# Optimization experiments

Measured on AMD Instinct MI355X. Metric: run time of the kernel, lower is better.

Reference implementation:

```python
import jax, jax.numpy as jnp
import numpy as np

B, S, H, I, E, TOP_K = 2, 1024, 1024, 2048, 8, 2


def setup_inputs() -> dict:
    key = jax.random.key(0)
    ks = jax.random.split(key, 5)
    return {
        "hidden_states": jax.random.normal(ks[0], (B, S, H), jnp.float32),
        # torch Linear weights are (out, in)
        "router_w": jax.random.normal(ks[1], (E, H), jnp.float32) * 0.02,
        "w1": jax.random.normal(ks[2], (E, I, H), jnp.float32) * 0.02,
        "v": jax.random.normal(ks[3], (E, I, H), jnp.float32) * 0.02,
        "w2": jax.random.normal(ks[4], (E, H, I), jnp.float32) * 0.02,
    }


def _moe(x, router_w, w1, v, w2):
    # x: [T, H] flattened tokens
    T = x.shape[0]
    n_exp = router_w.shape[0]
    logits = x @ router_w.T                                    # [T, E]
    probs = jax.nn.softmax(logits.astype(jnp.float32), axis=-1)
    top_p, top_i = jax.lax.top_k(probs, TOP_K)                 # [T, K]
    top_p = top_p / top_p.sum(axis=-1, keepdims=True)
    top_p = top_p.astype(x.dtype)
    # dense gate matrix [T, E]; zero for unselected experts -> identical math
    # to the torch gather / index_add combine
    gates = jnp.zeros((T, n_exp), x.dtype).at[
        jnp.arange(T)[:, None], top_i].set(top_p)
    out = jnp.zeros_like(x)
    for e in range(n_exp):  # small fixed expert loop keeps peak memory low
        h = jax.nn.gelu(x @ w1[e].T, approximate=False) * (x @ v[e].T)  # [T, I]
        out = out + gates[:, e:e + 1] * (h @ w2[e].T)                   # [T, H]
    return out, logits


def reference(hidden_states, router_w, w1, v, w2):
    b, s, h = hidden_states.shape
    out, logits = _moe(hidden_states.reshape(-1, h), router_w, w1, v, w2)
    return out.reshape(b, s, h), logits
```

## Files before the change

### kernel.cpp

```cpp
#include <hip/hip_runtime.h>
#include <math.h>

#define T 2048
#define HD 1024
#define ID 2048
#define NE 8
#define CSTRIDE 32

typedef short bf16x8 __attribute__((ext_vector_type(8)));
typedef float f32x4 __attribute__((ext_vector_type(4)));
typedef unsigned short u16x4 __attribute__((ext_vector_type(4)));
typedef unsigned short u16x8 __attribute__((ext_vector_type(8)));

__device__ __forceinline__ unsigned short f2bf(float f) {
  union { float f; unsigned u; } v; v.f = f;
  unsigned r = v.u + 0x7FFFu + ((v.u >> 16) & 1u);
  return (unsigned short)(r >> 16);
}

__device__ __forceinline__ u16x8 cvt8(float4 a, float4 b) {
  u16x8 o;
  o[0] = f2bf(a.x); o[1] = f2bf(a.y); o[2] = f2bf(a.z); o[3] = f2bf(a.w);
  o[4] = f2bf(b.x); o[5] = f2bf(b.y); o[6] = f2bf(b.z); o[7] = f2bf(b.w);
  return o;
}

__device__ __forceinline__ void cast_chunk16(const float* __restrict__ s,
                                             unsigned short* __restrict__ d,
                                             size_t base) {
  size_t o = base + (size_t)threadIdx.x * 4;
#pragma unroll
  for (int k = 0; k < 4; k++) {
    float4 f = *(const float4*)(s + o + k * 1024);
    u16x4 h;
    h[0] = f2bf(f.x); h[1] = f2bf(f.y); h[2] = f2bf(f.z); h[3] = f2bf(f.w);
    *(u16x4*)(d + o + k * 1024) = h;
  }
}

__device__ __forceinline__ void glds16(const unsigned short* g, unsigned short* l) {
  __builtin_amdgcn_global_load_lds(
      (const __attribute__((address_space(1))) unsigned int*)(g),
      (__attribute__((address_space(3))) unsigned int*)(l), 16, 0, 0);
}

__global__ __launch_bounds__(256) void prep_kernel(
    const float* __restrict__ x, const float* __restrict__ rw,
    unsigned short* __restrict__ xb, float* __restrict__ logits_out,
    int* __restrict__ pair_rowid, float* __restrict__ pair_gate,
    int* __restrict__ counts) {
  int bx = blockIdx.x;
  if (bx >= 256) {
    cast_chunk16(x, xb, (size_t)(bx - 256) * 4096);
    return;
  }
  __shared__ int s_e[16];
  __shared__ int s_rid[16];
  __shared__ float s_gt[16];
  int tid = threadIdx.x;
  int wid = tid >> 6, lane = tid & 63;
  for (int tk = 0; tk < 2; ++tk) {
    int t = bx * 8 + wid * 2 + tk;
    float acc[NE];
#pragma unroll
    for (int e = 0; e < NE; e++) acc[e] = 0.f;
    const float* xrow = x + (size_t)t * HD;
#pragma unroll 2
    for (int j = 0; j < HD; j += 64) {
      float xv = xrow[j + lane];
#pragma unroll
      for (int e = 0; e < NE; e++) acc[e] += xv * rw[e * HD + j + lane];
    }
#pragma unroll
    for (int e = 0; e < NE; e++)
      for (int off = 32; off > 0; off >>= 1) acc[e] += __shfl_xor(acc[e], off, 64);
    if (lane == 0) {
#pragma unroll
      for (int e = 0; e < NE; e++) logits_out[t * NE + e] = acc[e];
      int e0 = 0;
#pragma unroll
      for (int e = 1; e < NE; e++) if (acc[e] > acc[e0]) e0 = e;
      int e1 = (e0 == 0) ? 1 : 0;
#pragma unroll
      for (int e = 0; e < NE; e++)
        if (e != e0 && e != e1 && acc[e] > acc[e1]) e1 = e;
      float b = __expf(acc[e1] - acc[e0]);
      float g0 = 1.f / (1.f + b);
      float g1 = 1.f - g0;
      int slot = (wid * 2 + tk) * 2;
      s_e[slot] = e0; s_rid[slot] = t * 2;     s_gt[slot] = g0;
      s_e[slot + 1] = e1; s_rid[slot + 1] = t * 2 + 1; s_gt[slot + 1] = g1;
    }
  }
  __syncthreads();
  if (tid < NE) {
    int cnt = 0;
#pragma unroll
    for (int k = 0; k < 16; k++) if (s_e[k] == tid) cnt++;
    if (cnt) {
      int base = atomicAdd(&counts[tid * CSTRIDE], cnt);
      int p = 0;
      for (int k = 0; k < 16; k++)
        if (s_e[k] == tid) {
          pair_rowid[tid * T + base + p] = s_rid[k];
          pair_gate[tid * T + base + p] = s_gt[k];
          p++;
        }
    }
  }
}

__global__ __launch_bounds__(256) void gemm1_kernel(
    const unsigned short* __restrict__ xb, const float* __restrict__ w1,
    const float* __restrict__ v, unsigned short* __restrict__ hb,
    const int* __restrict__ pair_rowid, const int* __restrict__ counts) {
  int e = blockIdx.z;
  int cnt = counts[e * CSTRIDE];
  int row0 = blockIdx.y * 128;
  if (row0 >= cnt) return;
  __shared__ unsigned short As[2][128 * 64];
  __shared__ unsigned short B1s[2][64 * 64];
  __shared__ unsigned short B2s[2][64 * 64];
  int tid = threadIdx.x;
  int lane = tid & 63, wid = tid >> 6;
  int wr = wid >> 1, wc = wid & 1;
  int col0 = blockIdx.x * 64;
  int gr = lane >> 3, gc = lane & 7;
  const unsigned short *aA[4];
  const float *aB1[2], *aB2[2];
#pragma unroll
  for (int c = 0; c < 4; c++) {
    int row = (c * 4 + wid) * 8 + gr;
    int idx = row0 + row; if (idx > cnt - 1) idx = cnt - 1;
    int tok = pair_rowid[e * T + idx] >> 1;
    aA[c] = xb + (size_t)tok * HD + ((gc ^ (row & 7)) * 8);
  }
#pragma unroll
  for (int c = 0; c < 2; c++) {
    int row = (c * 4 + wid) * 8 + gr;
    int kswz = ((gc ^ (row & 7)) * 8);
    aB1[c] = w1 + ((size_t)(e * ID + col0 + row)) * HD + kswz;
    aB2[c] = v  + ((size_t)(e * ID + col0 + row)) * HD + kswz;
  }
  f32x4 acc1[4][2] = {};
  f32x4 acc3[4][2] = {};
  int mrow = lane & 15, kq = lane >> 4;
  int swzm = mrow & 7;
  float4 rb1[2][2], rb2[2][2];

  auto issue = [&](int buf, int kt) {
#pragma unroll
    for (int c = 0; c < 4; c++) glds16(aA[c] + kt, &As[buf][(c * 4 + wid) * 512]);
#pragma unroll
    for (int c = 0; c < 2; c++) {
      rb1[c][0] = *(const float4*)(aB1[c] + kt);
      rb1[c][1] = *(const float4*)(aB1[c] + kt + 4);
      rb2[c][0] = *(const float4*)(aB2[c] + kt);
      rb2[c][1] = *(const float4*)(aB2[c] + kt + 4);
    }
  };
  auto commitB = [&](int buf) {
#pragma unroll
    for (int c = 0; c < 2; c++) {
      *(u16x8*)&B1s[buf][(c * 4 + wid) * 512 + lane * 8] = cvt8(rb1[c][0], rb1[c][1]);
      *(u16x8*)&B2s[buf][(c * 4 + wid) * 512 + lane * 8] = cvt8(rb2[c][0], rb2[c][1]);
    }
  };
  auto compute = [&](int buf) {
#pragma unroll
    for (int kk = 0; kk < 2; kk++) {
      int g = kk * 4 + kq;
      int ko = ((g ^ swzm) * 8);
      bf16x8 a[4], b1[2], b2[2];
#pragma unroll
      for (int mi = 0; mi < 4; mi++)
        a[mi] = *(const bf16x8*)&As[buf][(wr * 64 + mi * 16 + mrow) * 64 + ko];
#pragma unroll
      for (int ni = 0; ni < 2; ni++) {
        b1[ni] = *(const bf16x8*)&B1s[buf][(wc * 32 + ni * 16 + mrow) * 64 + ko];
        b2[ni] = *(const bf16x8*)&B2s[buf][(wc * 32 + ni * 16 + mrow) * 64 + ko];
      }
#pragma unroll
      for (int mi = 0; mi < 4; mi++)
#pragma unroll
        for (int ni = 0; ni < 2; ni++) {
          acc1[mi][ni] = __builtin_amdgcn_mfma_f32_16x16x32_bf16(a[mi], b1[ni], acc1[mi][ni], 0, 0, 0);
          acc3[mi][ni] = __builtin_amdgcn_mfma_f32_16x16x32_bf16(a[mi], b2[ni], acc3[mi][ni], 0, 0, 0);
        }
    }
  };

  issue(0, 0);
  commitB(0);
  __syncthreads();
#pragma unroll 1
  for (int t = 0; t < 16; t += 2) {
    issue(1, (t + 1) * 64);
    compute(0);
    commitB(1);
    __syncthreads();
    if (t + 2 < 16) issue(0, (t + 2) * 64);
    compute(1);
    if (t + 2 < 16) commitB(0);
    __syncthreads();
  }

  int dcol = lane & 15, drow4 = (lane >> 4) * 4;
#pragma unroll
  for (int mi = 0; mi < 4; mi++)
#pragma unroll
    for (int ni = 0; ni < 2; ni++)
#pragma unroll
      for (int r = 0; r < 4; r++) {
        int lr = wr * 64 + mi * 16 + drow4 + r;
        if (row0 + lr < cnt) {
          float g1v = acc1[mi][ni][r];
          float g3v = acc3[mi][ni][r];
          float hval = 0.5f * g1v * (1.f + erff(g1v * 0.70710678118654752f)) * g3v;
          int rowid = pair_rowid[e * T + row0 + lr];
          hb[(size_t)rowid * ID + col0 + wc * 32 + ni * 16 + dcol] = f2bf(hval);
        }
      }
}

__global__ __launch_bounds__(256) void gemm2_kernel(
    const unsigned short* __restrict__ hb, const float* __restrict__ w2,
    float* __restrict__ yb, const int* __restrict__ pair_rowid,
    const float* __restrict__ pair_gate, const int* __restrict__ counts) {
  int e = blockIdx.z;
  int cnt = counts[e * CSTRIDE];
  int row0 = blockIdx.y * 128;
  if (row0 >= cnt) return;
  __shared__ unsigned short As[2][128 * 64];
  __shared__ unsigned short Bs[2][64 * 64];
  int tid = threadIdx.x;
  int lane = tid & 63, wid = tid >> 6;
  int wr = wid >> 1, wc = wid & 1;
  int col0 = blockIdx.x * 64;
  int gr = lane >> 3, gc = lane & 7;
  const unsigned short *aA[4];
  const float *aB[2];
#pragma unroll
  for (int c = 0; c < 4; c++) {
    int row = (c * 4 + wid) * 8 + gr;
    int idx = row0 + row; if (idx > cnt - 1) idx = cnt - 1;
    aA[c] = hb + (size_t)pair_rowid[e * T + idx] * ID + ((gc ^ (row & 7)) * 8);
  }
#pragma unroll
  for (int c = 0; c < 2; c++) {
    int row = (c * 4 + wid) * 8 + gr;
    int kswz = ((gc ^ (row & 7)) * 8);
    aB[c] = w2 + ((size_t)(e * HD + col0 + row)) * ID + kswz;
  }
  f32x4 acc[4][2] = {};
  int mrow = lane & 15, kq = lane >> 4;
  int swzm = mrow & 7;
  float4 rb[2][2];

  auto issue = [&](int buf, int kt) {
#pragma unroll
    for (int c = 0; c < 4; c++) glds16(aA[c] + kt, &As[buf][(c * 4 + wid) * 512]);
#pragma unroll
    for (int c = 0; c < 2; c++) {
      rb[c][0] = *(const float4*)(aB[c] + kt);
      rb[c][1] = *(const float4*)(aB[c] + kt + 4);
    }
  };
  auto commitB = [&](int buf) {
#pragma unroll
    for (int c = 0; c < 2; c++)
      *(u16x8*)&Bs[buf][(c * 4 + wid) * 512 + lane * 8] = cvt8(rb[c][0], rb[c][1]);
  };
  auto compute = [&](int buf) {
#pragma unroll
    for (int kk = 0; kk < 2; kk++) {
      int g = kk * 4 + kq;
      int ko = ((g ^ swzm) * 8);
      bf16x8 a[4], b[2];
#pragma unroll
      for (int mi = 0; mi < 4; mi++)
        a[mi] = *(const bf16x8*)&As[buf][(wr * 64 + mi * 16 + mrow) * 64 + ko];
#pragma unroll
      for (int ni = 0; ni < 2; ni++)
        b[ni] = *(const bf16x8*)&Bs[buf][(wc * 32 + ni * 16 + mrow) * 64 + ko];
#pragma unroll
      for (int mi = 0; mi < 4; mi++)
#pragma unroll
        for (int ni = 0; ni < 2; ni++)
          acc[mi][ni] = __builtin_amdgcn_mfma_f32_16x16x32_bf16(a[mi], b[ni], acc[mi][ni], 0, 0, 0);
    }
  };

  issue(0, 0);
  commitB(0);
  __syncthreads();
#pragma unroll 1
  for (int t = 0; t < 32; t += 2) {
    issue(1, (t + 1) * 64);
    compute(0);
    commitB(1);
    __syncthreads();
    if (t + 2 < 32) issue(0, (t + 2) * 64);
    compute(1);
    if (t + 2 < 32) commitB(0);
    __syncthreads();
  }

  int dcol = lane & 15, drow4 = (lane >> 4) * 4;
#pragma unroll
  for (int mi = 0; mi < 4; mi++)
#pragma unroll
    for (int ni = 0; ni < 2; ni++)
#pragma unroll
      for (int r = 0; r < 4; r++) {
        int lr = wr * 64 + mi * 16 + drow4 + r;
        if (row0 + lr < cnt) {
          float val = pair_gate[e * T + row0 + lr] * acc[mi][ni][r];
          yb[(size_t)pair_rowid[e * T + row0 + lr] * HD + col0 + wc * 32 + ni * 16 + dcol] = val;
        }
      }
}

__global__ __launch_bounds__(256) void combine_kernel(
    const float* __restrict__ yb, float* __restrict__ out) {
  size_t t = blockIdx.x;
  int c = threadIdx.x * 4;
  float4 a = *(const float4*)(yb + (t * 2) * HD + c);
  float4 b = *(const float4*)(yb + (t * 2 + 1) * HD + c);
  float4 o;
  o.x = a.x + b.x; o.y = a.y + b.y; o.z = a.z + b.z; o.w = a.w + b.w;
  *(float4*)(out + t * HD + c) = o;
}

extern "C" void kernel_launch(void* const* d_in, const int* in_sizes, int n_in,
                              void* d_out, int out_size, void* d_ws, size_t ws_size,
                              hipStream_t stream) {
  const float* x  = (const float*)d_in[0];
  const float* rw = (const float*)d_in[1];
  const float* w1 = (const float*)d_in[2];
  const float* v  = (const float*)d_in[3];
  const float* w2 = (const float*)d_in[4];
  float* out = (float*)d_out;
  float* logits_out = out + (size_t)T * HD;

  char* ws = (char*)d_ws;
  unsigned short* xb  = (unsigned short*)(ws);
  unsigned short* hb  = (unsigned short*)(ws + (4u << 20));
  float* yb           = (float*)(ws + (20u << 20));
  int*   pair_rowid   = (int*)  (ws + (116u << 20));
  float* pair_gate    = (float*)(ws + (116u << 20) + 65536);
  int*   counts       = (int*)  (ws + (116u << 20) + 131072);

  hipMemsetAsync(counts, 0, NE * CSTRIDE * sizeof(int), stream);

  prep_kernel<<<768, 256, 0, stream>>>(x, rw, xb, logits_out, pair_rowid,
                                       pair_gate, counts);
  gemm1_kernel<<<dim3(ID / 64, T / 128, NE), 256, 0, stream>>>(
      xb, w1, v, hb, pair_rowid, counts);
  gemm2_kernel<<<dim3(HD / 64, T / 128, NE), 256, 0, stream>>>(
      hb, w2, yb, pair_rowid, pair_gate, counts);
  combine_kernel<<<T, 256, 0, stream>>>(yb, out);
}
```

Before: 349.1 us.

## Replace async LDS double buffering with register-staged single-buffer pipeline in MoE GEMMs

Both expert GEMM kernels drop the global_load_lds direct-to-LDS path for the A tile and the double-buffered shared arrays. A and B tiles are now prefetched into registers during compute, then written to a single LDS buffer after a barrier. This halves LDS use per block, which could allow more resident blocks per CU, at the cost of an extra barrier per K step, more registers, and A data passing through VGPRs.

```diff
diff --git a/kernel.cpp b/kernel.cpp
--- a/kernel.cpp
+++ b/kernel.cpp
@@ -36,12 +36,6 @@
     h[0] = f2bf(f.x); h[1] = f2bf(f.y); h[2] = f2bf(f.z); h[3] = f2bf(f.w);
     *(u16x4*)(d + o + k * 1024) = h;
   }
-}
-
-__device__ __forceinline__ void glds16(const unsigned short* g, unsigned short* l) {
-  __builtin_amdgcn_global_load_lds(
-      (const __attribute__((address_space(1))) unsigned int*)(g),
-      (__attribute__((address_space(3))) unsigned int*)(l), 16, 0, 0);
 }
 
 __global__ __launch_bounds__(256) void prep_kernel(
@@ -118,9 +112,9 @@
   int cnt = counts[e * CSTRIDE];
   int row0 = blockIdx.y * 128;
   if (row0 >= cnt) return;
-  __shared__ unsigned short As[2][128 * 64];
-  __shared__ unsigned short B1s[2][64 * 64];
-  __shared__ unsigned short B2s[2][64 * 64];
+  __shared__ unsigned short As[128 * 64];
+  __shared__ unsigned short B1s[64 * 64];
+  __shared__ unsigned short B2s[64 * 64];
   int tid = threadIdx.x;
   int lane = tid & 63, wid = tid >> 6;
   int wr = wid >> 1, wc = wid & 1;
@@ -146,11 +140,12 @@
   f32x4 acc3[4][2] = {};
   int mrow = lane & 15, kq = lane >> 4;
   int swzm = mrow & 7;
+  u16x8 rA[4];
   float4 rb1[2][2], rb2[2][2];
 
-  auto issue = [&](int buf, int kt) {
-#pragma unroll
-    for (int c = 0; c < 4; c++) glds16(aA[c] + kt, &As[buf][(c * 4 + wid) * 512]);
+  auto loads = [&](int kt) {
+#pragma unroll
+    for (int c = 0; c < 4; c++) rA[c] = *(const u16x8*)(aA[c] + kt);
 #pragma unroll
     for (int c = 0; c < 2; c++) {
       rb1[c][0] = *(const float4*)(aB1[c] + kt);
@@ -159,14 +154,17 @@
       rb2[c][1] = *(const float4*)(aB2[c] + kt + 4);
     }
   };
-  auto commitB = [&](int buf) {
+  auto commit = [&]() {
+#pragma unroll
+    for (int c = 0; c < 4; c++)
+      *(u16x8*)&As[(c * 4 + wid) * 512 + lane * 8] = rA[c];
 #pragma unroll
     for (int c = 0; c < 2; c++) {
-      *(u16x8*)&B1s[buf][(c * 4 + wid) * 512 + lane * 8] = cvt8(rb1[c][0], rb1[c][1]);
-      *(u16x8*)&B2s[buf][(c * 4 + wid) * 512 + lane * 8] = cvt8(rb2[c][0], rb2[c][1]);
-    }
-  };
-  auto compute = [&](int buf) {
+      *(u16x8*)&B1s[(c * 4 + wid) * 512 + lane * 8] = cvt8(rb1[c][0], rb1[c][1]);
+      *(u16x8*)&B2s[(c * 4 + wid) * 512 + lane * 8] = cvt8(rb2[c][0], rb2[c][1]);
+    }
+  };
+  auto compute = [&]() {
 #pragma unroll
     for (int kk = 0; kk < 2; kk++) {
       int g = kk * 4 + kq;
@@ -174,11 +172,11 @@
       bf16x8 a[4], b1[2], b2[2];
 #pragma unroll
       for (int mi = 0; mi < 4; mi++)
-        a[mi] = *(const bf16x8*)&As[buf][(wr * 64 + mi * 16 + mrow) * 64 + ko];
+        a[mi] = *(const bf16x8*)&As[(wr * 64 + mi * 16 + mrow) * 64 + ko];
 #pragma unroll
       for (int ni = 0; ni < 2; ni++) {
-        b1[ni] = *(const bf16x8*)&B1s[buf][(wc * 32 + ni * 16 + mrow) * 64 + ko];
-        b2[ni] = *(const bf16x8*)&B2s[buf][(wc * 32 + ni * 16 + mrow) * 64 + ko];
+        b1[ni] = *(const bf16x8*)&B1s[(wc * 32 + ni * 16 + mrow) * 64 + ko];
+        b2[ni] = *(const bf16x8*)&B2s[(wc * 32 + ni * 16 + mrow) * 64 + ko];
       }
 #pragma unroll
       for (int mi = 0; mi < 4; mi++)
@@ -190,19 +188,15 @@
     }
   };
 
-  issue(0, 0);
-  commitB(0);
+  loads(0);
+  commit();
   __syncthreads();
 #pragma unroll 1
-  for (int t = 0; t < 16; t += 2) {
-    issue(1, (t + 1) * 64);
-    compute(0);
-    commitB(1);
+  for (int t = 0; t < 16; ++t) {
+    if (t < 15) loads((t + 1) * 64);
+    compute();
     __syncthreads();
-    if (t + 2 < 16) issue(0, (t + 2) * 64);
-    compute(1);
-    if (t + 2 < 16) commitB(0);
-    __syncthreads();
+    if (t < 15) { commit(); __syncthreads(); }
   }
 
   int dcol = lane & 15, drow4 = (lane >> 4) * 4;
@@ -231,8 +225,8 @@
   int cnt = counts[e * CSTRIDE];
   int row0 = blockIdx.y * 128;
   if (row0 >= cnt) return;
-  __shared__ unsigned short As[2][128 * 64];
-  __shared__ unsigned short Bs[2][64 * 64];
+  __shared__ unsigned short As[128 * 64];
+  __shared__ unsigned short Bs[64 * 64];
   int tid = threadIdx.x;
   int lane = tid & 63, wid = tid >> 6;
   int wr = wid >> 1, wc = wid & 1;
@@ -255,23 +249,27 @@
   f32x4 acc[4][2] = {};
   int mrow = lane & 15, kq = lane >> 4;
   int swzm = mrow & 7;
+  u16x8 rA[4];
   float4 rb[2][2];
 
-  auto issue = [&](int buf, int kt) {
-#pragma unroll
-    for (int c = 0; c < 4; c++) glds16(aA[c] + kt, &As[buf][(c * 4 + wid) * 512]);
+  auto loads = [&](int kt) {
+#pragma unroll
+    for (int c = 0; c < 4; c++) rA[c] = *(const u16x8*)(aA[c] + kt);
 #pragma unroll
     for (int c = 0; c < 2; c++) {
       rb[c][0] = *(const float4*)(aB[c] + kt);
       rb[c][1] = *(const float4*)(aB[c] + kt + 4);
     }
   };
-  auto commitB = [&](int buf) {
+  auto commit = [&]() {
+#pragma unroll
+    for (int c = 0; c < 4; c++)
+      *(u16x8*)&As[(c * 4 + wid) * 512 + lane * 8] = rA[c];
 #pragma unroll
     for (int c = 0; c < 2; c++)
-      *(u16x8*)&Bs[buf][(c * 4 + wid) * 512 + lane * 8] = cvt8(rb[c][0], rb[c][1]);
-  };
-  auto compute = [&](int buf) {
+      *(u16x8*)&Bs[(c * 4 + wid) * 512 + lane * 8] = cvt8(rb[c][0], rb[c][1]);
+  };
+  auto compute = [&]() {
 #pragma unroll
     for (int kk = 0; kk < 2; kk++) {
       int g = kk * 4 + kq;
@@ -279,10 +277,10 @@
       bf16x8 a[4], b[2];
 #pragma unroll
       for (int mi = 0; mi < 4; mi++)
-        a[mi] = *(const bf16x8*)&As[buf][(wr * 64 + mi * 16 + mrow) * 64 + ko];
+        a[mi] = *(const bf16x8*)&As[(wr * 64 + mi * 16 + mrow) * 64 + ko];
 #pragma unroll
       for (int ni = 0; ni < 2; ni++)
-        b[ni] = *(const bf16x8*)&Bs[buf][(wc * 32 + ni * 16 + mrow) * 64 + ko];
+        b[ni] = *(const bf16x8*)&Bs[(wc * 32 + ni * 16 + mrow) * 64 + ko];
 #pragma unroll
       for (int mi = 0; mi < 4; mi++)
 #pragma unroll
@@ -291,19 +289,15 @@
     }
   };
 
-  issue(0, 0);
-  commitB(0);
+  loads(0);
+  commit();
   __syncthreads();
 #pragma unroll 1
-  for (int t = 0; t < 32; t += 2) {
-    issue(1, (t + 1) * 64);
-    compute(0);
-    commitB(1);
+  for (int t = 0; t < 32; ++t) {
+    if (t < 31) loads((t + 1) * 64);
+    compute();
     __syncthreads();
-    if (t + 2 < 32) issue(0, (t + 2) * 64);
-    compute(1);
-    if (t + 2 < 32) commitB(0);
-    __syncthreads();
+    if (t < 31) { commit(); __syncthreads(); }
   }
 
   int dcol = lane & 15, drow4 = (lane >> 4) * 4;
```

Measured after the change: 349.5 us. Within noise of the previous version (+0.1%).
